# Kernel optimization log

Measured on AMD Instinct MI355X. Metric: run time of the kernel, lower is better.

Reference implementation:

```python
import jax, jax.numpy as jnp
import numpy as np

B, T, E, H = 8, 4096, 1024, 128

def setup_inputs() -> dict:
    key = jax.random.key(0)
    kx, kq, kk, kv = jax.random.split(key, 4)
    x = jax.random.normal(kx, (B, T, E), dtype=jnp.float32)
    # bias-free Linear weights stored as (in, out) for x @ W
    scale = 1.0 / np.sqrt(E)
    Wq = jax.random.normal(kq, (E, H), dtype=jnp.float32) * scale
    Wk = jax.random.normal(kk, (E, H), dtype=jnp.float32) * scale
    Wv = jax.random.normal(kv, (E, H), dtype=jnp.float32) * scale
    return {"x": x, "Wq": Wq, "Wk": Wk, "Wv": Wv}

def reference(x, Wq, Wk, Wv):
    # x: (B,T,E) -> out: (B,T,H). Causal single-head attention, dropout p=0 (no-op).
    q = x @ Wq  # (B,T,H)
    k = x @ Wk
    v = x @ Wv
    head_norm = jnp.sqrt(jnp.float32(q.shape[-1]))
    att = jnp.einsum('bth,bsh->bts', q, k) / head_norm  # (B,T,T)
    causal = jnp.tril(jnp.ones((x.shape[1], x.shape[1]), dtype=bool))
    att = jnp.where(causal, att, -jnp.inf)
    att = jax.nn.softmax(att, axis=-1)
    return jnp.einsum('bts,bsh->bth', att, v)
```

## Files before the change

kernel.cpp:

```cpp
#include <hip/hip_runtime.h>
#include <hip/hip_bf16.h>
#include <stdint.h>

#define Bn 8
#define Tn 4096
#define En 1024
#define Hn 128
#define SCALE 0.08838834764831845f

typedef __attribute__((ext_vector_type(8))) short bf16x8;
typedef __attribute__((ext_vector_type(4))) float f32x4;

__device__ __forceinline__ float bf2f(unsigned short v) {
    return __uint_as_float(((unsigned int)v) << 16);
}
__device__ __forceinline__ unsigned int pkbf(float a, float b) {
    __hip_bfloat162 h = __float22bfloat162_rn(make_float2(a, b));
    union { __hip_bfloat162 h2; unsigned int u; } cv;
    cv.h2 = h;
    return cv.u;
}

__device__ __forceinline__ void gll16(const unsigned short* g, unsigned short* l) {
    __builtin_amdgcn_global_load_lds(
        (const __attribute__((address_space(1))) void*)g,
        (__attribute__((address_space(3))) void*)l, 16, 0, 0);
}

__global__ __launch_bounds__(256)
void xcvt(const float* __restrict__ x, unsigned short* __restrict__ xb) {
    const size_t i = ((size_t)blockIdx.x * 256 + threadIdx.x) * 16;
    const float4* src = (const float4*)(x + i);
    float4 a = src[0], b = src[1], c = src[2], d = src[3];
    uint4 o0, o1;
    o0.x = pkbf(a.x, a.y); o0.y = pkbf(a.z, a.w);
    o0.z = pkbf(b.x, b.y); o0.w = pkbf(b.z, b.w);
    o1.x = pkbf(c.x, c.y); o1.y = pkbf(c.z, c.w);
    o1.z = pkbf(d.x, d.y); o1.w = pkbf(d.z, d.w);
    *(uint4*)(xb + i) = o0;
    *(uint4*)(xb + i + 8) = o1;
}

__global__ __launch_bounds__(256)
void wcvt(const float* __restrict__ Wq, const float* __restrict__ Wk,
          const float* __restrict__ Wv, unsigned short* __restrict__ wt3) {
    const int which = blockIdx.x;
    const int k0 = blockIdx.y * 128;
    const float* W = (which == 0) ? Wq : (which == 1) ? Wk : Wv;
    unsigned short* wt = wt3 + (size_t)which * 131072;

    __shared__ unsigned short wl[128 * 132];
    const int t = threadIdx.x;
#pragma unroll
    for (int i = 0; i < 16; ++i) {
        const int idx = t + i * 256;
        const int k = idx >> 5, c4 = idx & 31;
        float4 v = *(const float4*)&W[(size_t)(k0 + k) * Hn + c4 * 4];
        uint2 p;
        p.x = pkbf(v.x, v.y);
        p.y = pkbf(v.z, v.w);
        *(uint2*)&wl[k * 132 + c4 * 4] = p;
    }
    __syncthreads();
#pragma unroll
    for (int j = 0; j < 32; ++j) {
        const int idx = t + j * 256;
        const int n = idx >> 6, kp = idx & 63;
        unsigned int u = (unsigned int)wl[(2 * kp) * 132 + n] |
                         ((unsigned int)wl[(2 * kp + 1) * 132 + n] << 16);
        *(unsigned int*)&wt[(size_t)n * 1024 + k0 + 2 * kp] = u;
    }
}

#define QSWZ(r, c) (((r) << 7) + ((c) ^ (((r) & 7) << 4)))

__global__ __launch_bounds__(512, 4)
void qkv2(const unsigned short* __restrict__ xb,
          const unsigned short* __restrict__ wt3,
          unsigned short* __restrict__ Qo,
          unsigned short* __restrict__ Ko,
          unsigned short* __restrict__ Vo) {
    const int mt = blockIdx.x;
    const int which = blockIdx.y;
    const unsigned short* wt = wt3 + (size_t)which * 131072;
    unsigned short* out = (which == 0) ? Qo : (which == 1) ? Ko : Vo;
    const float scale = (which == 0) ? SCALE : 1.0f;

    __shared__ alignas(16) unsigned short Xs[2][128 * 64];
    __shared__ alignas(16) unsigned short Ws[2][128 * 64];

    const int t = threadIdx.x;
    const int w = t >> 6;
    const int lane = t & 63;
    const int quad = lane >> 4;
    const int l16 = lane & 15;
    const int r8 = lane >> 3;
    const int cb = lane & 7;

    const unsigned short* xtile = xb + (size_t)(mt * 128) * En;

    f32x4 acc[8];
#pragma unroll
    for (int nst = 0; nst < 8; ++nst) acc[nst] = (f32x4){0.f, 0.f, 0.f, 0.f};

    auto stage = [&](int buf, int kt) {
#pragma unroll
        for (int i = 0; i < 2; ++i) {
            const int row = w * 16 + i * 8 + r8;
            gll16(xtile + (size_t)row * En + kt * 64 + ((cb ^ (row & 7)) * 8),
                  &Xs[buf][(w * 16 + i * 8) * 64]);
        }
#pragma unroll
        for (int i = 0; i < 2; ++i) {
            const int row = w * 16 + i * 8 + r8;
            gll16(wt + (size_t)row * 1024 + kt * 64 + ((cb ^ (row & 7)) * 8),
                  &Ws[buf][(w * 16 + i * 8) * 64]);
        }
    };

    stage(0, 0);
    __syncthreads();

    for (int kt = 0; kt < 16; ++kt) {
        const int buf = kt & 1;
        if (kt < 15) stage(buf ^ 1, kt + 1);
        const char* xs = (const char*)Xs[buf];
        const char* ws = (const char*)Ws[buf];
#pragma unroll
        for (int ks = 0; ks < 2; ++ks) {
            bf16x8 af = *(const bf16x8*)(xs + QSWZ(w * 16 + l16, ks * 64 + quad * 16));
#pragma unroll
            for (int nst = 0; nst < 8; ++nst) {
                bf16x8 bfr = *(const bf16x8*)(ws + QSWZ(nst * 16 + l16, ks * 64 + quad * 16));
                acc[nst] = __builtin_amdgcn_mfma_f32_16x16x32_bf16(bfr, af, acc[nst], 0, 0, 0);
            }
        }
        if (kt < 15) __syncthreads();
    }

    {
        const size_t rowbase = (size_t)(mt * 128 + w * 16 + l16) * Hn;
#pragma unroll
        for (int nst = 0; nst < 8; ++nst) {
            f32x4 v = acc[nst];
            uint2 pk;
            pk.x = pkbf(v[0] * scale, v[1] * scale);
            pk.y = pkbf(v[2] * scale, v[3] * scale);
            *(uint2*)(out + rowbase + nst * 16 + quad * 4) = pk;
        }
    }
}

__global__ __launch_bounds__(256)
void qkv_mfma(const float* __restrict__ x,
              const float* __restrict__ Wq,
              const float* __restrict__ Wk,
              const float* __restrict__ Wv,
              unsigned short* __restrict__ Qo,
              unsigned short* __restrict__ Ko,
              unsigned short* __restrict__ Vo) {
    const int mt = blockIdx.x;
    const int which = blockIdx.y;
    const float* W = (which == 0) ? Wq : (which == 1) ? Wk : Wv;
    unsigned short* out = (which == 0) ? Qo : (which == 1) ? Ko : Vo;
    const float scale = (which == 0) ? SCALE : 1.0f;

    __shared__ alignas(16) unsigned short Xs[128 * 72];
    __shared__ alignas(16) unsigned short Wt[128 * 72];

    const int t = threadIdx.x;
    const int w = t >> 6;
    const int lane = t & 63;
    const int quad = lane >> 4;
    const int l16 = lane & 15;

    const int xrow = t >> 1;
    const int xkc = (t & 1) * 32;
    const int ws0 = (t & 31) * 2;
    const int wd0 = (t >> 5) * 16;

    const float* xsrc0 = x + (size_t)(mt * 128 + xrow) * En + xkc;

    f32x4 acc[2][8];
#pragma unroll
    for (int mi = 0; mi < 2; ++mi)
#pragma unroll
        for (int nst = 0; nst < 8; ++nst) acc[mi][nst] = (f32x4){0.f, 0.f, 0.f, 0.f};

    float4 xpre[8], wpre[8];
    {
        const float* src = xsrc0;
#pragma unroll
        for (int i = 0; i < 8; ++i) xpre[i] = *(const float4*)(src + i * 4);
        const float* w0 = W + (size_t)ws0 * Hn + wd0;
        const float* w1 = w0 + Hn;
#pragma unroll
        for (int i = 0; i < 4; ++i) wpre[i] = *(const float4*)(w0 + i * 4);
#pragma unroll
        for (int i = 0; i < 4; ++i) wpre[4 + i] = *(const float4*)(w1 + i * 4);
    }

    for (int kt = 0; kt < 16; ++kt) {
        __syncthreads();
        {
            unsigned int u[16];
#pragma unroll
            for (int i = 0; i < 8; ++i) {
                u[2 * i]     = pkbf(xpre[i].x, xpre[i].y);
                u[2 * i + 1] = pkbf(xpre[i].z, xpre[i].w);
            }
#pragma unroll
            for (int i = 0; i < 4; ++i)
                *(uint4*)&Xs[xrow * 72 + xkc + i * 8] = ((const uint4*)u)[i];

            const float* ax = (const float*)&wpre[0];
            const float* bx = (const float*)&wpre[4];
#pragma unroll
            for (int dd = 0; dd < 16; ++dd)
                *(unsigned int*)&Wt[(wd0 + dd) * 72 + ws0] = pkbf(ax[dd], bx[dd]);
        }
        if (kt < 15) {
            const float* src = xsrc0 + (kt + 1) * 64;
#pragma unroll
            for (int i = 0; i < 8; ++i) xpre[i] = *(const float4*)(src + i * 4);
            const float* w0 = W + (size_t)((kt + 1) * 64 + ws0) * Hn + wd0;
            const float* w1 = w0 + Hn;
#pragma unroll
            for (int i = 0; i < 4; ++i) wpre[i] = *(const float4*)(w0 + i * 4);
#pragma unroll
            for (int i = 0; i < 4; ++i) wpre[4 + i] = *(const float4*)(w1 + i * 4);
        }
        __syncthreads();

#pragma unroll
        for (int ks = 0; ks < 2; ++ks) {
            bf16x8 af[2];
#pragma unroll
            for (int mi = 0; mi < 2; ++mi)
                af[mi] = *(const bf16x8*)&Xs[(w * 32 + mi * 16 + l16) * 72 + ks * 32 + quad * 8];
#pragma unroll
            for (int nst = 0; nst < 8; ++nst) {
                bf16x8 bfr = *(const bf16x8*)&Wt[(nst * 16 + l16) * 72 + ks * 32 + quad * 8];
                acc[0][nst] = __builtin_amdgcn_mfma_f32_16x16x32_bf16(bfr, af[0], acc[0][nst], 0, 0, 0);
                acc[1][nst] = __builtin_amdgcn_mfma_f32_16x16x32_bf16(bfr, af[1], acc[1][nst], 0, 0, 0);
            }
        }
    }

#pragma unroll
    for (int mi = 0; mi < 2; ++mi) {
        const size_t rowbase = (size_t)(mt * 128 + w * 32 + mi * 16 + l16) * Hn;
#pragma unroll
        for (int nst = 0; nst < 8; ++nst) {
            f32x4 v = acc[mi][nst];
            uint2 pk;
            pk.x = pkbf(v[0] * scale, v[1] * scale);
            pk.y = pkbf(v[2] * scale, v[3] * scale);
            *(uint2*)(out + rowbase + nst * 16 + quad * 4) = pk;
        }
    }
}

#define KSWZ(r, c) (((r) << 8) + ((c) ^ (((r) & 7) << 4)))
#define VSWZ(r, c) (((r) << 7) + ((c) ^ (((r) & 7) << 4)))

__global__ __launch_bounds__(512, 4)
void flash_mfma(const unsigned short* __restrict__ Qb,
                const unsigned short* __restrict__ Kb,
                const unsigned short* __restrict__ Vb,
                float* __restrict__ out) {
    const int b = blockIdx.x;
    const int bx = blockIdx.y;
    const int qt = (bx < 32) ? (63 - bx) : (bx - 32);
    const int t = threadIdx.x;
    const int w = t >> 6;
    const int g = w >> 2;
    const int rg = w & 3;
    const int lane = t & 63;
    const int quad = lane >> 4;
    const int l16 = lane & 15;
    const int t256 = t & 255;

    extern __shared__ unsigned short pool[];
    char* const poolb = (char*)pool;
    char* const Kg = poolb + g * 16384;
    char* const Vg = poolb + 32768 + g * 16384;
    char* const Pw = poolb + 65536 + w * 2048;
    float* const Os = (float*)poolb;
    float* const Ex = (float*)(poolb + 40960);
    float* const Em = (float*)(poolb + 73728);
    float* const El = Em + 64;

    const size_t gbase = (size_t)b * ((size_t)Tn * Hn);
    const unsigned short* kbase = Kb + gbase;
    const unsigned short* vbase = Vb + gbase;

    const int l_hi = lane >> 4;
    const int cpr = (lane & 15) * 16;
    const int vs0 = (t256 & 31) * 2;
    const int vd0 = (t256 >> 5) * 16;

    uint4 vra, vrb, vrc, vrd;
    if (g <= qt) {
        const unsigned short* vsrc = vbase + (size_t)(g * 64) * Hn;
        vra = *(const uint4*)&vsrc[vs0 * 128 + vd0];
        vrb = *(const uint4*)&vsrc[vs0 * 128 + vd0 + 8];
        vrc = *(const uint4*)&vsrc[(vs0 + 1) * 128 + vd0];
        vrd = *(const uint4*)&vsrc[(vs0 + 1) * 128 + vd0 + 8];
    }

    {
        const unsigned short* qsrc = Qb + gbase + (size_t)(qt * 64) * Hn;
#pragma unroll
        for (int i = 0; i < 2; ++i) {
            const int row = w * 8 + i * 4 + l_hi;
            const int scol = cpr ^ ((row & 7) << 4);
            gll16(qsrc + row * 128 + (scol >> 1),
                  (unsigned short*)(poolb + w * 2048 + i * 1024));
        }
    }
    __syncthreads();

    bf16x8 qf[4];
#pragma unroll
    for (int ks = 0; ks < 4; ++ks)
        qf[ks] = *(const bf16x8*)(poolb + KSWZ(rg * 16 + l16, ks * 64 + quad * 16));

    f32x4 acc_o[8];
#pragma unroll
    for (int i = 0; i < 8; ++i) acc_o[i] = (f32x4){0.f, 0.f, 0.f, 0.f};
    float m_run = -1e30f, l_run = 0.f;

    const int n = (qt >> 1) + 1;
    for (int it = 0; it < n; ++it) {
        const int kt = 2 * it + g;
        const bool active = (kt <= qt);
        __syncthreads();
        if (active) {
            const unsigned short* ktile = kbase + (size_t)(kt * 64) * Hn;
#pragma unroll
            for (int i = 0; i < 4; ++i) {
                const int row = rg * 16 + i * 4 + l_hi;
                const int scol = cpr ^ ((row & 7) << 4);
                gll16(ktile + row * 128 + (scol >> 1),
                      (unsigned short*)(Kg + rg * 4096 + i * 1024));
            }
            const unsigned short* pa = (const unsigned short*)&vra;
            const unsigned short* pb = (const unsigned short*)&vrb;
            const unsigned short* pc = (const unsigned short*)&vrc;
            const unsigned short* pd = (const unsigned short*)&vrd;
#pragma unroll
            for (int dd = 0; dd < 8; ++dd)
                *(unsigned int*)(Vg + VSWZ(vd0 + dd, vs0 * 2)) =
                    (unsigned int)pa[dd] | ((unsigned int)pc[dd] << 16);
#pragma unroll
            for (int dd = 0; dd < 8; ++dd)
                *(unsigned int*)(Vg + VSWZ(vd0 + 8 + dd, vs0 * 2)) =
                    (unsigned int)pb[dd] | ((unsigned int)pd[dd] << 16);
        }
        __syncthreads();
        if (kt + 2 <= qt) {
            const unsigned short* vsrc = vbase + (size_t)((kt + 2) * 64) * Hn;
            vra = *(const uint4*)&vsrc[vs0 * 128 + vd0];
            vrb = *(const uint4*)&vsrc[vs0 * 128 + vd0 + 8];
            vrc = *(const uint4*)&vsrc[(vs0 + 1) * 128 + vd0];
            vrd = *(const uint4*)&vsrc[(vs0 + 1) * 128 + vd0 + 8];
        }
        if (!active) continue;

        const bool diag = (kt == qt);
        f32x4 sa[4];
#pragma unroll
        for (int st = 0; st < 4; ++st) {
            if (diag && st > rg) {
                sa[st] = (f32x4){-1e30f, -1e30f, -1e30f, -1e30f};
            } else {
                f32x4 c = (f32x4){0.f, 0.f, 0.f, 0.f};
#pragma unroll
                for (int ks = 0; ks < 4; ++ks) {
                    bf16x8 kf = *(const bf16x8*)(Kg + KSWZ(st * 16 + l16, ks * 64 + quad * 16));
                    c = __builtin_amdgcn_mfma_f32_16x16x32_bf16(kf, qf[ks], c, 0, 0, 0);
                }
                if (diag && st == rg) {
#pragma unroll
                    for (int r = 0; r < 4; ++r)
                        if (quad * 4 + r > l16) c[r] = -1e30f;
                }
                sa[st] = c;
            }
        }

        float t0 = fmaxf(fmaxf(sa[0][0], sa[0][1]), fmaxf(sa[0][2], sa[0][3]));
        float t1 = fmaxf(fmaxf(sa[1][0], sa[1][1]), fmaxf(sa[1][2], sa[1][3]));
        float t2 = fmaxf(fmaxf(sa[2][0], sa[2][1]), fmaxf(sa[2][2], sa[2][3]));
        float t3 = fmaxf(fmaxf(sa[3][0], sa[3][1]), fmaxf(sa[3][2], sa[3][3]));
        float mloc = fmaxf(fmaxf(t0, t1), fmaxf(t2, t3));
        mloc = fmaxf(mloc, __shfl_xor(mloc, 16));
        mloc = fmaxf(mloc, __shfl_xor(mloc, 32));

        if (!__all(mloc <= m_run + 8.0f)) {
            const float m_new = fmaxf(m_run, mloc);
            const float alpha = __expf(m_run - m_new);
            l_run *= alpha;
#pragma unroll
            for (int i = 0; i < 8; ++i) acc_o[i] *= alpha;
            m_run = m_new;
        }
        float lsum = 0.f;
#pragma unroll
        for (int st = 0; st < 4; ++st)
#pragma unroll
            for (int r = 0; r < 4; ++r) {
                const float e = __expf(sa[st][r] - m_run);
                sa[st][r] = e;
                lsum += e;
            }
        lsum += __shfl_xor(lsum, 16);
        lsum += __shfl_xor(lsum, 32);
        l_run += lsum;

#pragma unroll
        for (int st = 0; st < 4; ++st) {
            uint2 pk;
            pk.x = pkbf(sa[st][0], sa[st][1]);
            pk.y = pkbf(sa[st][2], sa[st][3]);
            *(uint2*)(Pw + VSWZ(l16, st * 32 + quad * 8)) = pk;
        }
        bf16x8 pf0 = *(const bf16x8*)(Pw + VSWZ(l16, quad * 16));
        bf16x8 pf1 = *(const bf16x8*)(Pw + VSWZ(l16, 64 + quad * 16));

#pragma unroll
        for (int dt = 0; dt < 8; ++dt) {
            bf16x8 vf0 = *(const bf16x8*)(Vg + VSWZ(dt * 16 + l16, quad * 16));
            acc_o[dt] = __builtin_amdgcn_mfma_f32_16x16x32_bf16(vf0, pf0, acc_o[dt], 0, 0, 0);
            bf16x8 vf1 = *(const bf16x8*)(Vg + VSWZ(dt * 16 + l16, 64 + quad * 16));
            acc_o[dt] = __builtin_amdgcn_mfma_f32_16x16x32_bf16(vf1, pf1, acc_o[dt], 0, 0, 0);
        }
    }

    __syncthreads();
    if (g == 1) {
        float* dst = Ex + (rg * 16 + l16) * 128;
#pragma unroll
        for (int dt = 0; dt < 8; ++dt)
            *(f32x4*)&dst[dt * 16 + quad * 4] = acc_o[dt];
        if (quad == 0) {
            Em[rg * 16 + l16] = m_run;
            El[rg * 16 + l16] = l_run;
        }
    }
    __syncthreads();
    if (g == 0) {
        const float* src = Ex + (rg * 16 + l16) * 128;
        const float m2 = Em[rg * 16 + l16];
        const float l2 = El[rg * 16 + l16];
        const float ms = fmaxf(m_run, m2);
        const float a1 = __expf(m_run - ms);
        const float a2 = __expf(m2 - ms);
        const float linv = 1.f / (l_run * a1 + l2 * a2);
#pragma unroll
        for (int dt = 0; dt < 8; ++dt) {
            f32x4 o2 = *(const f32x4*)&src[dt * 16 + quad * 4];
            f32x4 v = (acc_o[dt] * a1 + o2 * a2) * linv;
            *(f32x4*)&Os[(rg * 16 + l16) * 132 + dt * 16 + quad * 4] = v;
        }
    }
    __syncthreads();
    float* dst = out + gbase + (size_t)(qt * 64) * Hn;
#pragma unroll
    for (int i = 0; i < 4; ++i) {
        const int idx = (t + i * 512) * 4;
        const int row = idx >> 7, col = idx & 127;
        *(float4*)&dst[row * 128 + col] = *(const float4*)&Os[row * 132 + col];
    }
}

extern "C" void kernel_launch(void* const* d_in, const int* in_sizes, int n_in,
                              void* d_out, int out_size, void* d_ws, size_t ws_size,
                              hipStream_t stream) {
    const float* x  = (const float*)d_in[0];
    const float* Wq = (const float*)d_in[1];
    const float* Wk = (const float*)d_in[2];
    const float* Wv = (const float*)d_in[3];
    float* o = (float*)d_out;

    const size_t qkvb = (size_t)Bn * Tn * Hn;
    unsigned short* Qb = (unsigned short*)d_ws;
    unsigned short* Kb = Qb + qkvb;
    unsigned short* Vb = Kb + qkvb;
    unsigned short* xbf = Vb + qkvb;
    unsigned short* wt3 = xbf + (size_t)Bn * Tn * En;

    const size_t ws_need = (3 * qkvb + (size_t)Bn * Tn * En + 3 * (size_t)Hn * En)
                           * sizeof(unsigned short);

    static bool attr_done = false;
    if (!attr_done) {
        hipFuncSetAttribute((const void*)flash_mfma,
                            hipFuncAttributeMaxDynamicSharedMemorySize, 81920);
        attr_done = true;
    }

    if (ws_size >= ws_need) {
        xcvt<<<8192, 256, 0, stream>>>(x, xbf);
        wcvt<<<dim3(3, 8), 256, 0, stream>>>(Wq, Wk, Wv, wt3);
        qkv2<<<dim3(256, 3), 512, 0, stream>>>(xbf, wt3, Qb, Kb, Vb);
    } else {
        qkv_mfma<<<dim3(256, 3), 256, 0, stream>>>(x, Wq, Wk, Wv, Qb, Kb, Vb);
    }
    flash_mfma<<<dim3(8, 64), 512, 81920, stream>>>(Qb, Kb, Vb, o);
}
```

Baseline: 346.9 us.

## Split causal attention KV range across two blocks and merge partials

Result: no change. 341.4 us, median of 2 (-1.6%).

```diff
diff --git a/kernel.cpp b/kernel.cpp
--- a/kernel.cpp
+++ b/kernel.cpp
@@ -268,10 +268,18 @@
 void flash_mfma(const unsigned short* __restrict__ Qb,
                 const unsigned short* __restrict__ Kb,
                 const unsigned short* __restrict__ Vb,
-                float* __restrict__ out) {
+                float* __restrict__ out,
+                float* __restrict__ Up,
+                float2* __restrict__ MLp) {
     const int b = blockIdx.x;
     const int bx = blockIdx.y;
     const int qt = (bx < 32) ? (63 - bx) : (bx - 32);
+    const int z = blockIdx.z;
+    const bool split = (gridDim.z == 2);
+    const int h0 = (qt + 2) >> 1;
+    const int lo = (split && z) ? h0 : 0;
+    const int hi = split ? (z ? (qt + 1) : h0) : (qt + 1);
+    const int R = hi - lo;
     const int t = threadIdx.x;
     const int w = t >> 6;
     const int g = w >> 2;
@@ -301,8 +309,8 @@
     const int vd0 = (t256 >> 5) * 16;
 
     uint4 vra, vrb, vrc, vrd;
-    if (g <= qt) {
-        const unsigned short* vsrc = vbase + (size_t)(g * 64) * Hn;
+    if (lo + g < hi) {
+        const unsigned short* vsrc = vbase + (size_t)((lo + g) * 64) * Hn;
         vra = *(const uint4*)&vsrc[vs0 * 128 + vd0];
         vrb = *(const uint4*)&vsrc[vs0 * 128 + vd0 + 8];
         vrc = *(const uint4*)&vsrc[(vs0 + 1) * 128 + vd0];
@@ -331,10 +339,10 @@
     for (int i = 0; i < 8; ++i) acc_o[i] = (f32x4){0.f, 0.f, 0.f, 0.f};
     float m_run = -1e30f, l_run = 0.f;
 
-    const int n = (qt >> 1) + 1;
+    const int n = (R + 1) >> 1;
     for (int it = 0; it < n; ++it) {
-        const int kt = 2 * it + g;
-        const bool active = (kt <= qt);
+        const int kt = lo + 2 * it + g;
+        const bool active = (kt < hi);
         __syncthreads();
         if (active) {
             const unsigned short* ktile = kbase + (size_t)(kt * 64) * Hn;
@@ -359,7 +367,7 @@
                     (unsigned int)pb[dd] | ((unsigned int)pd[dd] << 16);
         }
         __syncthreads();
-        if (kt + 2 <= qt) {
+        if (kt + 2 < hi) {
             const unsigned short* vsrc = vbase + (size_t)((kt + 2) * 64) * Hn;
             vra = *(const uint4*)&vsrc[vs0 * 128 + vd0];
             vrb = *(const uint4*)&vsrc[vs0 * 128 + vd0 + 8];
@@ -457,22 +465,46 @@
         const float ms = fmaxf(m_run, m2);
         const float a1 = __expf(m_run - ms);
         const float a2 = __expf(m2 - ms);
-        const float linv = 1.f / (l_run * a1 + l2 * a2);
+        const float den = l_run * a1 + l2 * a2;
+        const float scl = split ? 1.f : (1.f / den);
 #pragma unroll
         for (int dt = 0; dt < 8; ++dt) {
             f32x4 o2 = *(const f32x4*)&src[dt * 16 + quad * 4];
-            f32x4 v = (acc_o[dt] * a1 + o2 * a2) * linv;
+            f32x4 v = (acc_o[dt] * a1 + o2 * a2) * scl;
             *(f32x4*)&Os[(rg * 16 + l16) * 132 + dt * 16 + quad * 4] = v;
         }
+        if (split && quad == 0)
+            MLp[(size_t)z * (Bn * Tn) + (size_t)b * Tn + qt * 64 + rg * 16 + l16] =
+                make_float2(ms, den);
     }
     __syncthreads();
-    float* dst = out + gbase + (size_t)(qt * 64) * Hn;
+    float* dst = split
+        ? (Up + ((size_t)z * Bn * Tn + (size_t)b * Tn + (size_t)qt * 64) * Hn)
+        : (out + gbase + (size_t)(qt * 64) * Hn);
 #pragma unroll
     for (int i = 0; i < 4; ++i) {
         const int idx = (t + i * 512) * 4;
         const int row = idx >> 7, col = idx & 127;
         *(float4*)&dst[row * 128 + col] = *(const float4*)&Os[row * 132 + col];
     }
+}
+
+__global__ __launch_bounds__(256)
+void fcomb(const float* __restrict__ U, const float2* __restrict__ ml,
+           float* __restrict__ out) {
+    const size_t i = (size_t)blockIdx.x * 256 + threadIdx.x;
+    const size_t grow = i >> 5;
+    const int c4 = (int)(i & 31) * 4;
+    const float2 p0 = ml[grow];
+    const float2 p1 = ml[(size_t)Bn * Tn + grow];
+    const float ms = fmaxf(p0.x, p1.x);
+    const float a0 = __expf(p0.x - ms);
+    const float a1 = __expf(p1.x - ms);
+    const float inv = 1.f / (a0 * p0.y + a1 * p1.y);
+    const f32x4 u0 = *(const f32x4*)&U[grow * Hn + c4];
+    const f32x4 u1 = *(const f32x4*)&U[(size_t)Bn * Tn * Hn + grow * Hn + c4];
+    f32x4 v = (u0 * a0 + u1 * a1) * inv;
+    *(f32x4*)&out[grow * Hn + c4] = v;
 }
 
 extern "C" void kernel_launch(void* const* d_in, const int* in_sizes, int n_in,
@@ -491,6 +523,9 @@
     unsigned short* xbf = Vb + qkvb;
     unsigned short* wt3 = xbf + (size_t)Bn * Tn * En;
 
+    float* Up = (float*)xbf;
+    float2* MLp = (float2*)((char*)xbf + (size_t)2 * Bn * Tn * Hn * sizeof(float));
+
     const size_t ws_need = (3 * qkvb + (size_t)Bn * Tn * En + 3 * (size_t)Hn * En)
                            * sizeof(unsigned short);
 
@@ -505,8 +540,11 @@
         xcvt<<<8192, 256, 0, stream>>>(x, xbf);
         wcvt<<<dim3(3, 8), 256, 0, stream>>>(Wq, Wk, Wv, wt3);
         qkv2<<<dim3(256, 3), 512, 0, stream>>>(xbf, wt3, Qb, Kb, Vb);
+        flash_mfma<<<dim3(8, 64, 2), 512, 81920, stream>>>(Qb, Kb, Vb, o, Up, MLp);
+        fcomb<<<4096, 256, 0, stream>>>(Up, MLp, o);
     } else {
         qkv_mfma<<<dim3(256, 3), 256, 0, stream>>>(x, Wq, Wk, Wv, Qb, Kb, Vb);
-    }
-    flash_mfma<<<dim3(8, 64), 512, 81920, stream>>>(Qb, Kb, Vb, o);
-}
+        flash_mfma<<<dim3(8, 64, 1), 512, 81920, stream>>>(Qb, Kb, Vb, o,
+                                                           nullptr, nullptr);
+    }
+}
```
